# Performance work log

Measured on AMD Instinct MI355X. Metric: run time of the kernel, lower is better.

The kernel has to match this reference:

```python
import jax, jax.numpy as jnp
import numpy as np

STRIDES = (8, 16, 32, 64, 128)
HW = ((100, 128), (50, 64), (25, 32), (13, 16), (7, 8))
NUM_CLASSES = 80
SCORE_THR = 0.05
IOU_THR = 0.6
MAX_NUM = 1000


def _flatten(x):
    # [B,C,H,W] -> [B,H*W,C]  (matches reshape_feats)
    B, C, H, W = x.shape
    return jnp.transpose(x, (0, 2, 3, 1)).reshape(B, H * W, C)


def _coords():
    # center coordinates of every FPN location in input-image scale, concatenated over levels -> [N,2] (x,y)
    cs = []
    for (h, w), s in zip(HW, STRIDES):
        xs = jnp.arange(w, dtype=jnp.float32) * s + s // 2
        ys = jnp.arange(h, dtype=jnp.float32) * s + s // 2
        yy, xx = jnp.meshgrid(ys, xs, indexing='ij')
        cs.append(jnp.stack([xx.reshape(-1), yy.reshape(-1)], axis=-1))
    return jnp.concatenate(cs, axis=0)


def _iou_matrix(boxes):
    # boxes [N,4] (x1,y1,x2,y2) -> pairwise IoU [N,N]
    x1, y1, x2, y2 = jnp.split(boxes, 4, axis=-1)  # each [N,1]
    area = jnp.clip(x2 - x1, 0.0) * jnp.clip(y2 - y1, 0.0)
    ix1 = jnp.maximum(x1, x1.T)
    iy1 = jnp.maximum(y1, y1.T)
    ix2 = jnp.minimum(x2, x2.T)
    iy2 = jnp.minimum(y2, y2.T)
    inter = jnp.clip(ix2 - ix1, 0.0) * jnp.clip(iy2 - iy1, 0.0)
    union = area + area.T - inter
    return inter / jnp.maximum(union, 1e-9)


def _nms_single(scores, labels, boxes):
    # Per-image class-aware greedy NMS on topk candidates; returns fixed-size padded
    # (scores, labels, boxes, keep_mask) where suppressed/below-thr entries have keep=False.
    valid = scores > SCORE_THR  # score_mask from _post_process
    s = jnp.where(valid, scores, -1.0)
    order = jnp.argsort(-s)
    s = s[order]
    lb = labels[order]
    bx = boxes[order]
    valid = valid[order]
    # class-offset trick from _batch_nms: offset boxes per label by (coord_max + 1)
    coord_max = jnp.max(jnp.where(valid[:, None], bx, 0.0))
    off = lb.astype(bx.dtype) * (coord_max + 1.0)
    iou = _iou_matrix(bx + off[:, None])
    N = s.shape[0]
    idx = jnp.arange(N)

    def body(i, keep):
        sup = keep[i] & (iou[i] > IOU_THR) & (idx > i)
        return keep & jnp.logical_not(sup)

    keep = jax.lax.fori_loop(0, N, body, valid)
    return jnp.where(keep, s, 0.0), jnp.where(keep, lb, 0), bx, keep


def setup_inputs() -> dict:
    key = jax.random.key(0)
    ks = jax.random.split(key, 15)
    inp = {}
    i = 0
    for name, c, scale in (('cls', NUM_CLASSES, None), ('reg', 4, 128.0), ('ctr', 1, None)):
        for lvl, (h, w) in zip((3, 4, 5, 6, 7), HW):
            if scale is None:
                x = jax.random.normal(ks[i], (16, c, h, w), dtype=jnp.float32)
            else:
                x = jax.random.uniform(ks[i], (16, c, h, w), dtype=jnp.float32) * scale
            inp[f'{name}_p{lvl}'] = x
            i += 1
    return inp


def reference(cls_p3, cls_p4, cls_p5, cls_p6, cls_p7,
              reg_p3, reg_p4, reg_p5, reg_p6, reg_p7,
              ctr_p3, ctr_p4, ctr_p5, ctr_p6, ctr_p7):
    cls = jnp.concatenate([_flatten(t) for t in (cls_p3, cls_p4, cls_p5, cls_p6, cls_p7)], axis=1)  # [B,N,80]
    reg = jnp.concatenate([_flatten(t) for t in (reg_p3, reg_p4, reg_p5, reg_p6, reg_p7)], axis=1)  # [B,N,4]
    ctr = jnp.concatenate([_flatten(t) for t in (ctr_p3, ctr_p4, ctr_p5, ctr_p6, ctr_p7)], axis=1)  # [B,N,1]

    cls_preds = jax.nn.sigmoid(cls)
    ctr_preds = jax.nn.sigmoid(ctr)[..., 0]
    cls_scores = jnp.max(cls_preds, axis=-1)
    pred_labels = jnp.argmax(cls_preds, axis=-1) + 1  # labels start at 1
    cls_scores = jnp.sqrt(cls_scores * ctr_preds)  # use_ctr=True fusion

    coords = _coords()  # [N,2]
    pred_boxes = jnp.concatenate([coords - reg[..., :2], coords + reg[..., 2:]], axis=-1)  # [B,N,4]

    topk_s, topk_i = jax.lax.top_k(cls_scores, MAX_NUM)
    topk_l = jnp.take_along_axis(pred_labels, topk_i, axis=1)
    topk_b = jnp.take_along_axis(pred_boxes, topk_i[..., None], axis=1)

    return jax.vmap(_nms_single)(topk_s, topk_l, topk_b)
```

## Files before the change

kernel.cpp:

```cpp
#include <hip/hip_runtime.h>
#include <cstdint>


typedef unsigned long long ull;

#define BATCH 16
#define NLOC 17064
#define NPAD 18432
#define NCHUNK 9
#define CHUNK 2048
#define TOPK 1000
#define TOPKP 1024
#define NCLS 80
#define SCORE_THR 0.05f
#define IOU_THR 0.6f

struct Ptrs { const float* cls[5]; const float* reg[5]; const float* ctr[5]; };

__global__ __launch_bounds__(256) void score_kernel(Ptrs p, ull* __restrict__ keys,
                                                    int* __restrict__ labels,
                                                    float* __restrict__ boxes) {
  int idx = blockIdx.x * 256 + threadIdx.x;
  if (idx >= BATCH * NPAD) return;
  int b = idx / NPAD, n = idx - b * NPAD;
  if (n >= NLOC) { keys[idx] = 0ull; return; }

  int lvl, off, lw, st, H;
  if (n < 12800)      { lvl=0; off=0;     lw=7; st=8;   H=100; }
  else if (n < 16000) { lvl=1; off=12800; lw=6; st=16;  H=50;  }
  else if (n < 16800) { lvl=2; off=16000; lw=5; st=32;  H=25;  }
  else if (n < 17008) { lvl=3; off=16800; lw=4; st=64;  H=13;  }
  else                { lvl=4; off=17008; lw=3; st=128; H=7;   }
  int hw = n - off;
  int w = hw & ((1 << lw) - 1), h = hw >> lw;
  int HW = H << lw;
  float fs = (float)st, half = fs * 0.5f;
  float x = (float)w * fs + half, y = (float)h * fs + half;

  const float* cb = p.cls[lvl] + (size_t)b * NCLS * HW + hw;
  float best = cb[0]; int bi = 0;
  for (int c = 1; c < NCLS; ++c) {
    float v = cb[(size_t)c * HW];
    if (v > best) { best = v; bi = c; }
  }
  const float* rb = p.reg[lvl] + (size_t)b * 4 * HW + hw;
  float r0 = rb[0], r1 = rb[HW], r2 = rb[2 * (size_t)HW], r3 = rb[3 * (size_t)HW];
  float ct = p.ctr[lvl][(size_t)b * HW + hw];

  float pcls = 1.f / (1.f + expf(-best));
  float pctr = 1.f / (1.f + expf(-ct));
  float score = sqrtf(pcls * pctr);

  keys[idx] = ((ull)__float_as_uint(score) << 32) | (ull)(0xFFFFFFFFu - (unsigned)n);
  labels[(size_t)b * NLOC + n] = bi + 1;
  float* bx = boxes + ((size_t)b * NLOC + n) * 4;
  bx[0] = x - r0; bx[1] = y - r1; bx[2] = x + r2; bx[3] = y + r3;
}

__global__ __launch_bounds__(512) void chunk_sort_kernel(const ull* __restrict__ keys,
                                                         ull* __restrict__ runs) {
  __shared__ ull s[CHUNK];
  int b = blockIdx.x / NCHUNK, c = blockIdx.x % NCHUNK;
  const ull* src = keys + (size_t)b * NPAD + (size_t)c * CHUNK;
  for (int i = threadIdx.x; i < CHUNK; i += 512) s[i] = src[i];
  __syncthreads();
  for (int k = 2; k <= CHUNK; k <<= 1) {
    for (int j = k >> 1; j > 0; j >>= 1) {
      for (int t = threadIdx.x; t < CHUNK / 2; t += 512) {
        int i = ((t & ~(j - 1)) << 1) | (t & (j - 1));
        int ixj = i | j;
        bool desc = (i & k) == 0;
        ull a = s[i], bb = s[ixj];
        bool sw = desc ? (a < bb) : (a > bb);
        if (sw) { s[i] = bb; s[ixj] = a; }
      }
      __syncthreads();
    }
  }
  ull* dst = runs + ((size_t)b * NCHUNK + c) * TOPKP;
  for (int i = threadIdx.x; i < TOPKP; i += 512) dst[i] = s[i];
}

__global__ __launch_bounds__(512) void merge_level_kernel(const ull* __restrict__ src,
    ull* __restrict__ dst, int npairs, int carry, int srcRPI, int dstRPI) {
  int per = npairs + carry;
  int b = blockIdx.x / per, p = blockIdx.x % per;
  const ull* sb = src + (size_t)b * srcRPI * TOPKP;
  ull* db = dst + (size_t)b * dstRPI * TOPKP;
  int tid = threadIdx.x;
  if (p >= npairs) {
    for (int i = tid; i < TOPKP; i += 512)
      db[(size_t)p * TOPKP + i] = sb[(size_t)(2 * npairs) * TOPKP + i];
    return;
  }
  __shared__ ull m[TOPKP];
  const ull* A = sb + (size_t)(2 * p) * TOPKP;
  const ull* B = sb + (size_t)(2 * p + 1) * TOPKP;
  for (int i = tid; i < TOPKP; i += 512) {
    ull a = A[i], c = B[TOPKP - 1 - i];
    m[i] = a > c ? a : c;
  }
  __syncthreads();
  for (int j = TOPKP / 2; j > 0; j >>= 1) {
    for (int t = tid; t < TOPKP / 2; t += 512) {
      int i = ((t & ~(j - 1)) << 1) | (t & (j - 1));
      int ixj = i | j;
      ull a = m[i], c = m[ixj];
      if (a < c) { m[i] = c; m[ixj] = a; }
    }
    __syncthreads();
  }
  for (int i = tid; i < TOPKP; i += 512) db[(size_t)p * TOPKP + i] = m[i];
}

__global__ __launch_bounds__(256) void gather_kernel(const ull* __restrict__ topkeys,
    const int* __restrict__ labels, const float* __restrict__ boxes,
    float* __restrict__ topS, int* __restrict__ topL, float* __restrict__ topOB,
    ull* __restrict__ validWords, float* __restrict__ outBoxes) {
  __shared__ float red[256];
  __shared__ float s_cmax;
  int b = blockIdx.x, tid = threadIdx.x;
  float lmax = 0.f;
  for (int k = tid; k < TOPKP; k += 256) {
    ull key = topkeys[(size_t)b * TOPKP + k];
    float sc = 0.f; int lb = 0;
    float b0 = 0.f, b1 = 0.f, b2 = 0.f, b3 = 0.f;
    bool inR = (k < TOPK);
    if (inR) {
      sc = __uint_as_float((unsigned)(key >> 32));
      unsigned n = 0xFFFFFFFFu - (unsigned)(key & 0xFFFFFFFFull);
      lb = labels[(size_t)b * NLOC + n];
      const float* bp = boxes + ((size_t)b * NLOC + n) * 4;
      b0 = bp[0]; b1 = bp[1]; b2 = bp[2]; b3 = bp[3];
      float* ob = outBoxes + ((size_t)b * TOPK + k) * 4;
      ob[0] = b0; ob[1] = b1; ob[2] = b2; ob[3] = b3;
    }
    topS[(size_t)b * TOPKP + k] = sc;
    topL[(size_t)b * TOPKP + k] = lb;
    float* tb = topOB + ((size_t)b * TOPKP + k) * 4;
    tb[0] = b0; tb[1] = b1; tb[2] = b2; tb[3] = b3;
    bool valid = inR && (sc > SCORE_THR);
    if (valid) lmax = fmaxf(lmax, fmaxf(fmaxf(b0, b1), fmaxf(b2, b3)));
    ull vb = __ballot(valid ? 1 : 0);
    if ((tid & 63) == 0) validWords[b * 16 + (k >> 6)] = vb;
  }
  red[tid] = lmax;
  __syncthreads();
  for (int sft = 128; sft > 0; sft >>= 1) {
    if (tid < sft) red[tid] = fmaxf(red[tid], red[tid + sft]);
    __syncthreads();
  }
  if (tid == 0) s_cmax = red[0];
  __syncthreads();
  float offb = s_cmax + 1.0f;
  for (int k = tid; k < TOPKP; k += 256) {
    float off = (float)topL[(size_t)b * TOPKP + k] * offb;
    float* tb = topOB + ((size_t)b * TOPKP + k) * 4;
    tb[0] += off; tb[1] += off; tb[2] += off; tb[3] += off;
  }
}

__global__ __launch_bounds__(1024) void sup_kernel(const float* __restrict__ topOB,
                                                   ull* __restrict__ sup) {
  int bid = blockIdx.x;
  int b = bid / TOPK, i = bid - b * TOPK;
  int j = threadIdx.x;
  const float4* OB = (const float4*)topOB + (size_t)b * TOPKP;
  float4 A = OB[i];
  float aw = fmaxf(A.z - A.x, 0.f), ah = fmaxf(A.w - A.y, 0.f);
  float areaA = aw * ah;
  bool bit = false;
  if (j > i && j < TOPK) {
    float4 Bx = OB[j];
    float bw = fmaxf(Bx.z - Bx.x, 0.f), bh = fmaxf(Bx.w - Bx.y, 0.f);
    float areaB = bw * bh;
    float ix1 = fmaxf(A.x, Bx.x), iy1 = fmaxf(A.y, Bx.y);
    float ix2 = fminf(A.z, Bx.z), iy2 = fminf(A.w, Bx.w);
    float inter = fmaxf(ix2 - ix1, 0.f) * fmaxf(iy2 - iy1, 0.f);
    float uni = areaA + areaB - inter;
    float iou = inter / fmaxf(uni, 1e-9f);
    bit = iou > IOU_THR;
  }
  ull m = __ballot(bit ? 1 : 0);
  if ((j & 63) == 0) sup[((size_t)b * TOPKP + i) * 16 + (j >> 6)] = m;
}

#define CS(K) { unsigned rl = __builtin_amdgcn_readlane(dlo, (K));             \
    unsigned rh = __builtin_amdgcn_readlane(dhi, (K));                         \
    ull take = (M >> (K)) & 1ull; ull msk = 0ull - take;                       \
    M &= ~((((ull)rh << 32) | (ull)rl) & msk); km |= take << (K); }
#define CS8(B8) CS((B8)+0) CS((B8)+1) CS((B8)+2) CS((B8)+3) CS((B8)+4)         \
    CS((B8)+5) CS((B8)+6) CS((B8)+7)

__global__ __launch_bounds__(256) void nms_scan_kernel(const ull* __restrict__ sup,
    const ull* __restrict__ validWords, const float* __restrict__ topS,
    const int* __restrict__ topL, float* __restrict__ out) {
  __shared__ ull ls[2][2048];
  __shared__ ull dgls[2][128];
  int b = blockIdx.x, tid = threadIdx.x;
  int wave = tid >> 6, lane = tid & 63;
  const ull* S = sup + (size_t)b * TOPKP * 16;

  for (int k = 0; k < 8; ++k) {
    int j = tid + 256 * k;
    ull v = S[j];
    ls[0][j] = v;
    if ((j & 15) == (j >> 10)) dgls[0][j >> 4] = v;
  }
  ull rm = 0xFFFFFFFFFFFFFFFFull;
  if (wave == 0 && lane < 16) rm = ~validWords[b * 16 + lane];
  __syncthreads();

  for (int g = 0; g < 8; ++g) {
    if (wave > 0 && g < 7) {
      const ull* src = S + (size_t)(g + 1) * 2048;
      ull* dst = ls[(g + 1) & 1];
      ull* ddst = dgls[(g + 1) & 1];
      int base = 2 * (g + 1);
      for (int j = tid - 64; j < 2048; j += 192) {
        ull v = src[j];
        dst[j] = v;
        if ((j & 15) == base + (j >> 10)) ddst[j >> 4] = v;
      }
    }
    if (wave == 0) {
      const ull* B = ls[g & 1];
      const ull* D = dgls[g & 1];
      int lg = lane >> 4, wd = lane & 15;
      for (int wl = 0; wl < 2; ++wl) {
        int w = 2 * g + wl;
        ull dg = D[wl * 64 + lane];
        unsigned dlo = (unsigned)dg, dhi = (unsigned)(dg >> 32);
        unsigned mlo = __builtin_amdgcn_readlane((unsigned)rm, w);
        unsigned mhi = __builtin_amdgcn_readlane((unsigned)(rm >> 32), w);
        ull M = ~(((ull)mhi << 32) | (ull)mlo);
        ull km = 0;
        CS8(0) CS8(8) CS8(16) CS8(24) CS8(32) CS8(40) CS8(48) CS8(56)
        const ull* RB = B + (size_t)(wl * 64 + lg) * 16 + wd;
        ull accB = 0;
#pragma unroll
        for (int t = 0; t < 16; ++t) {
          ull bit = (km >> (4 * t + lg)) & 1ull;
          accB |= RB[(size_t)t * 64] & (0ull - bit);
        }
        accB |= __shfl_xor(accB, 16);
        accB |= __shfl_xor(accB, 32);
        rm |= accB;
      }
    }
    __syncthreads();
  }

  if (wave == 0) {
    ull keep_na = ~rm;
    const float* tS = topS + (size_t)b * TOPKP;
    const int*   tL = topL + (size_t)b * TOPKP;
    float* outS = out;
    float* outL = out + BATCH * TOPK;
    float* outK = out + BATCH * TOPK * 6;
    for (int t = 0; t < 16; ++t) {
      int j = t * 64 + lane;
      ull kw = __shfl(keep_na, t);
      if (j < TOPK) {
        bool kp = (kw >> lane) & 1ull;
        outS[(size_t)b * TOPK + j] = kp ? tS[j] : 0.f;
        outL[(size_t)b * TOPK + j] = kp ? (float)tL[j] : 0.f;
        outK[(size_t)b * TOPK + j] = kp ? 1.f : 0.f;
      }
    }
  }
}
#undef CS8
#undef CS

extern "C" void kernel_launch(void* const* d_in, const int* in_sizes, int n_in,
                              void* d_out, int out_size, void* d_ws, size_t ws_size,
                              hipStream_t stream) {
  Ptrs p;
  for (int l = 0; l < 5; ++l) {
    p.cls[l] = (const float*)d_in[l];
    p.reg[l] = (const float*)d_in[5 + l];
    p.ctr[l] = (const float*)d_in[10 + l];
  }
  char* ws = (char*)d_ws;
  size_t o = 0;
  auto alloc = [&](size_t bytes) -> void* {
    void* r = ws + o; o += (bytes + 255) & ~(size_t)255; return r;
  };
  ull*   keys       = (ull*)  alloc((size_t)BATCH * NPAD * 8);
  int*   labels     = (int*)  alloc((size_t)BATCH * NLOC * 4);
  float* boxes      = (float*)alloc((size_t)BATCH * NLOC * 16);
  ull*   runs       = (ull*)  alloc((size_t)BATCH * NCHUNK * TOPKP * 8);
  ull*   runs2      = (ull*)  alloc((size_t)BATCH * NCHUNK * TOPKP * 8);
  ull*   topkeys    = (ull*)  alloc((size_t)BATCH * TOPKP * 8);
  float* topS       = (float*)alloc((size_t)BATCH * TOPKP * 4);
  int*   topL       = (int*)  alloc((size_t)BATCH * TOPKP * 4);
  float* topOB      = (float*)alloc((size_t)BATCH * TOPKP * 16);
  ull*   validWords = (ull*)  alloc((size_t)BATCH * 16 * 8);
  ull*   sup        = (ull*)  alloc((size_t)BATCH * TOPKP * 16 * 8);

  float* out = (float*)d_out;
  float* outBoxes = out + 2 * BATCH * TOPK;

  hipLaunchKernelGGL(score_kernel, dim3((BATCH * NPAD + 255) / 256), dim3(256), 0, stream,
                     p, keys, labels, boxes);
  hipLaunchKernelGGL(chunk_sort_kernel, dim3(BATCH * NCHUNK), dim3(512), 0, stream,
                     keys, runs);
  hipLaunchKernelGGL(merge_level_kernel, dim3(BATCH * 5), dim3(512), 0, stream,
                     runs, runs2, 4, 1, NCHUNK, NCHUNK);
  hipLaunchKernelGGL(merge_level_kernel, dim3(BATCH * 3), dim3(512), 0, stream,
                     runs2, runs, 2, 1, NCHUNK, NCHUNK);
  hipLaunchKernelGGL(merge_level_kernel, dim3(BATCH * 2), dim3(512), 0, stream,
                     runs, runs2, 1, 1, NCHUNK, NCHUNK);
  hipLaunchKernelGGL(merge_level_kernel, dim3(BATCH * 1), dim3(512), 0, stream,
                     runs2, topkeys, 1, 0, NCHUNK, 1);
  hipLaunchKernelGGL(gather_kernel, dim3(BATCH), dim3(256), 0, stream,
                     topkeys, labels, boxes, topS, topL, topOB, validWords, outBoxes);
  hipLaunchKernelGGL(sup_kernel, dim3(BATCH * TOPK), dim3(1024), 0, stream,
                     topOB, sup);
  hipLaunchKernelGGL(nms_scan_kernel, dim3(BATCH), dim3(256), 0, stream,
                     sup, validWords, topS, topL, out);
}
```

Measured before the change: 254.4 us.

## Prefetch next NMS mask chunk into registers across all waves during scan

The NMS scan kernel now has all four waves, including the scanning wave, issue global loads of the next 2048-word suppression-mask chunk into registers before the scan. They write the chunk to the shared-memory double buffer only after the scan finishes. A sched_barrier keeps the loads ahead of the scan. The separate diagonal-block shared array is removed, and the diagonal words are read directly from the main buffer. The aim is to hide global-load latency behind the serial bit scan and to shorten the strided copy loop, at the cost of more registers on wave 0.

```diff
diff --git a/kernel.cpp b/kernel.cpp
--- a/kernel.cpp
+++ b/kernel.cpp
@@ -196,47 +196,47 @@
     const ull* __restrict__ validWords, const float* __restrict__ topS,
     const int* __restrict__ topL, float* __restrict__ out) {
   __shared__ ull ls[2][2048];
-  __shared__ ull dgls[2][128];
   int b = blockIdx.x, tid = threadIdx.x;
   int wave = tid >> 6, lane = tid & 63;
   const ull* S = sup + (size_t)b * TOPKP * 16;
 
-  for (int k = 0; k < 8; ++k) {
-    int j = tid + 256 * k;
-    ull v = S[j];
-    ls[0][j] = v;
-    if ((j & 15) == (j >> 10)) dgls[0][j >> 4] = v;
-  }
   ull rm = 0xFFFFFFFFFFFFFFFFull;
   if (wave == 0 && lane < 16) rm = ~validWords[b * 16 + lane];
+
+  {
+    ull s0 = S[tid], s1 = S[tid + 256], s2 = S[tid + 512], s3 = S[tid + 768],
+        s4 = S[tid + 1024], s5 = S[tid + 1280], s6 = S[tid + 1536],
+        s7 = S[tid + 1792];
+    ls[0][tid] = s0;        ls[0][tid + 256] = s1;  ls[0][tid + 512] = s2;
+    ls[0][tid + 768] = s3;  ls[0][tid + 1024] = s4; ls[0][tid + 1280] = s5;
+    ls[0][tid + 1536] = s6; ls[0][tid + 1792] = s7;
+  }
   __syncthreads();
 
   for (int g = 0; g < 8; ++g) {
-    if (wave > 0 && g < 7) {
+    ull s0 = 0, s1 = 0, s2 = 0, s3 = 0, s4 = 0, s5 = 0, s6 = 0, s7 = 0;
+    bool st = (g < 7);
+    if (st) {
       const ull* src = S + (size_t)(g + 1) * 2048;
-      ull* dst = ls[(g + 1) & 1];
-      ull* ddst = dgls[(g + 1) & 1];
-      int base = 2 * (g + 1);
-      for (int j = tid - 64; j < 2048; j += 192) {
-        ull v = src[j];
-        dst[j] = v;
-        if ((j & 15) == base + (j >> 10)) ddst[j >> 4] = v;
-      }
-    }
+      s0 = src[tid];        s1 = src[tid + 256];  s2 = src[tid + 512];
+      s3 = src[tid + 768];  s4 = src[tid + 1024]; s5 = src[tid + 1280];
+      s6 = src[tid + 1536]; s7 = src[tid + 1792];
+    }
+    __builtin_amdgcn_sched_barrier(0);
+
     if (wave == 0) {
-      const ull* B = ls[g & 1];
-      const ull* D = dgls[g & 1];
+      const ull* Bf = ls[g & 1];
       int lg = lane >> 4, wd = lane & 15;
       for (int wl = 0; wl < 2; ++wl) {
         int w = 2 * g + wl;
-        ull dg = D[wl * 64 + lane];
+        ull dg = Bf[(size_t)(wl * 64 + lane) * 16 + w];
         unsigned dlo = (unsigned)dg, dhi = (unsigned)(dg >> 32);
         unsigned mlo = __builtin_amdgcn_readlane((unsigned)rm, w);
         unsigned mhi = __builtin_amdgcn_readlane((unsigned)(rm >> 32), w);
         ull M = ~(((ull)mhi << 32) | (ull)mlo);
         ull km = 0;
         CS8(0) CS8(8) CS8(16) CS8(24) CS8(32) CS8(40) CS8(48) CS8(56)
-        const ull* RB = B + (size_t)(wl * 64 + lg) * 16 + wd;
+        const ull* RB = Bf + (size_t)(wl * 64 + lg) * 16 + wd;
         ull accB = 0;
 #pragma unroll
         for (int t = 0; t < 16; ++t) {
@@ -247,6 +247,13 @@
         accB |= __shfl_xor(accB, 32);
         rm |= accB;
       }
+    }
+
+    if (st) {
+      ull* dst = ls[(g + 1) & 1];
+      dst[tid] = s0;        dst[tid + 256] = s1;  dst[tid + 512] = s2;
+      dst[tid + 768] = s3;  dst[tid + 1024] = s4; dst[tid + 1280] = s5;
+      dst[tid + 1536] = s6; dst[tid + 1792] = s7;
     }
     __syncthreads();
   }
```

After: 253.5 us. No clear change (-0.3%).
